# Performance work log

Measured on AMD Instinct MI355X. Metric: run time of the kernel, lower is better.

Reference implementation:

```python
import jax, jax.numpy as jnp
import numpy as np

EPS = 1e-5
D_MODEL, D_INNER, D_STATE, DT_RANK, D_CONV = 768, 1536, 16, 48, 4
B, T, FREQ, CLASSES = 4, 1000, 229, 88
MIDFEAT = 128 * (FREQ // 16)  # 1792


def conv2d_same(x, w):
    return jax.lax.conv_general_dilated(x, w, (1, 1), 'SAME',
                                        dimension_numbers=('NCHW', 'OIHW', 'NCHW'))


def bn2d_eval(h, g, b):
    # eval-mode BatchNorm2d with running_mean=0, running_var=1 (init values)
    s = g / jnp.sqrt(1.0 + EPS)
    return h * s[None, :, None, None] + b[None, :, None, None]


def conv_block(h, w1, g1, b1, w2, g2, b2):
    h = jax.nn.relu(bn2d_eval(conv2d_same(h, w1), g1, b1))
    h = jax.nn.relu(bn2d_eval(conv2d_same(h, w2), g2, b2))
    # avg_pool2d kernel (1,2), stride (1,2), floor mode -> VALID reduce_window
    h = jax.lax.reduce_window(h, 0.0, jax.lax.add, (1, 1, 1, 2), (1, 1, 1, 2), 'VALID')
    return h * 0.5


def mamba(x, in_w, conv_w, conv_b, xproj_w, dt_w, dt_b, A_log, Dp, out_w):
    Bb, L, _ = x.shape
    xz = x @ in_w.T                                  # (B,L,2*d_inner)
    xm, z = xz[..., :D_INNER], xz[..., D_INNER:]
    # depthwise causal conv1d, kernel 4, left pad 3
    xt = jax.lax.conv_general_dilated(xm.transpose(0, 2, 1), conv_w, (1,),
                                      [(D_CONV - 1, 0)],
                                      dimension_numbers=('NCH', 'OIH', 'NCH'),
                                      feature_group_count=D_INNER)
    xm = jax.nn.silu(xt.transpose(0, 2, 1) + conv_b)  # (B,L,d_inner)
    dbl = xm @ xproj_w.T                              # (B,L,dt_rank+2*d_state)
    dt = jax.nn.softplus(dbl[..., :DT_RANK] @ dt_w.T + dt_b)   # (B,L,d_inner)
    Bm = dbl[..., DT_RANK:DT_RANK + D_STATE]          # (B,L,N)
    Cm = dbl[..., DT_RANK + D_STATE:]                 # (B,L,N)
    A = -jnp.exp(A_log)                               # (d_inner,N)
    dA = jnp.exp(jnp.einsum('bld,dn->bldn', dt, A))   # (B,L,d_inner,N)
    dBx = jnp.einsum('bld,bln->bldn', dt * xm, Bm)    # (B,L,d_inner,N)

    def step(h, inp):
        a, bx, c = inp
        h = a * h + bx                                # (B,d_inner,N)
        return h, jnp.einsum('bdn,bn->bd', h, c)

    h0 = jnp.zeros((Bb, D_INNER, D_STATE), x.dtype)
    _, ys = jax.lax.scan(step, h0, (dA.transpose(1, 0, 2, 3),
                                    dBx.transpose(1, 0, 2, 3),
                                    Cm.transpose(1, 0, 2)))
    y = ys.transpose(1, 0, 2) + xm * Dp               # (B,L,d_inner)
    return (y * jax.nn.silu(z)) @ out_w.T             # (B,L,d_model)


def _forward(x,
             cb1_w1, cb1_g1, cb1_b1, cb1_w2, cb1_g2, cb1_b2,
             cb2_w1, cb2_g1, cb2_b1, cb2_w2, cb2_g2, cb2_b2,
             cb3_w1, cb3_g1, cb3_b1, cb3_w2, cb3_g2, cb3_b2,
             cb4_w1, cb4_g1, cb4_b1, cb4_w2, cb4_g2, cb4_b2,
             fc5_w, bn5_g, bn5_b, ln_g, ln_b,
             m_in_w, m_conv_w, m_conv_b, m_xproj_w, m_dt_w, m_dt_b,
             m_A_log, m_D, m_out_w, proj_w, proj_b):
    h = conv_block(x, cb1_w1, cb1_g1, cb1_b1, cb1_w2, cb1_g2, cb1_b2)
    h = conv_block(h, cb2_w1, cb2_g1, cb2_b1, cb2_w2, cb2_g2, cb2_b2)
    h = conv_block(h, cb3_w1, cb3_g1, cb3_b1, cb3_w2, cb3_g2, cb3_b2)
    h = conv_block(h, cb4_w1, cb4_g1, cb4_b1, cb4_w2, cb4_g2, cb4_b2)
    Bb, C, Tt, Fq = h.shape                           # (B,128,T,14)
    h = h.transpose(0, 2, 1, 3).reshape(Bb, Tt, C * Fq)  # torch transpose(1,2).flatten(2)
    # fc5 (bias=False) + eval BatchNorm1d(768) + relu
    h = jax.nn.relu((h @ fc5_w.T) * (bn5_g / jnp.sqrt(1.0 + EPS)) + bn5_b)
    mu = h.mean(-1, keepdims=True)
    var = ((h - mu) ** 2).mean(-1, keepdims=True)
    h = (h - mu) / jnp.sqrt(var + EPS) * ln_g + ln_b
    h = mamba(h, m_in_w, m_conv_w, m_conv_b, m_xproj_w, m_dt_w, m_dt_b,
              m_A_log, m_D, m_out_w)
    return jax.nn.sigmoid(h @ proj_w.T + proj_b)      # (B,T,classes)


def setup_inputs() -> dict:
    key = jax.random.key(0)
    ks = iter(jax.random.split(key, 64))

    def rn(shape, s=0.02):
        return jax.random.normal(next(ks), shape, jnp.float32) * s

    d = {'x': jax.random.normal(next(ks), (B, 1, T, FREQ), jnp.float32)}
    for i, (ci, co) in enumerate([(1, 48), (48, 64), (64, 96), (96, 128)], 1):
        d[f'cb{i}_w1'] = rn((co, ci, 3, 3), 0.1)
        d[f'cb{i}_g1'] = jnp.ones((co,), jnp.float32)
        d[f'cb{i}_b1'] = jnp.zeros((co,), jnp.float32)
        d[f'cb{i}_w2'] = rn((co, co, 3, 3), 0.05)
        d[f'cb{i}_g2'] = jnp.ones((co,), jnp.float32)
        d[f'cb{i}_b2'] = jnp.zeros((co,), jnp.float32)
    d['fc5_w'] = rn((D_MODEL, MIDFEAT))
    d['bn5_g'] = jnp.ones((D_MODEL,), jnp.float32)
    d['bn5_b'] = jnp.zeros((D_MODEL,), jnp.float32)
    d['ln_g'] = jnp.ones((D_MODEL,), jnp.float32)
    d['ln_b'] = jnp.zeros((D_MODEL,), jnp.float32)
    d['m_in_w'] = rn((2 * D_INNER, D_MODEL))
    d['m_conv_w'] = rn((D_INNER, 1, D_CONV), 0.1)
    d['m_conv_b'] = jnp.zeros((D_INNER,), jnp.float32)
    d['m_xproj_w'] = rn((DT_RANK + 2 * D_STATE, D_INNER))
    d['m_dt_w'] = rn((D_INNER, DT_RANK), 0.05)
    d['m_dt_b'] = jax.random.uniform(next(ks), (D_INNER,), jnp.float32, -6.0, -3.0)
    d['m_A_log'] = jnp.log(jnp.tile(jnp.arange(1, D_STATE + 1, dtype=jnp.float32)[None, :],
                                    (D_INNER, 1)))
    d['m_D'] = jnp.ones((D_INNER,), jnp.float32)
    d['m_out_w'] = rn((D_MODEL, D_INNER))
    d['proj_w'] = rn((CLASSES, D_MODEL))
    d['proj_b'] = jnp.zeros((CLASSES,), jnp.float32)
    return d


def reference(x,
              cb1_w1, cb1_g1, cb1_b1, cb1_w2, cb1_g2, cb1_b2,
              cb2_w1, cb2_g1, cb2_b1, cb2_w2, cb2_g2, cb2_b2,
              cb3_w1, cb3_g1, cb3_b1, cb3_w2, cb3_g2, cb3_b2,
              cb4_w1, cb4_g1, cb4_b1, cb4_w2, cb4_g2, cb4_b2,
              fc5_w, bn5_g, bn5_b, ln_g, ln_b,
              m_in_w, m_conv_w, m_conv_b, m_xproj_w, m_dt_w, m_dt_b,
              m_A_log, m_D, m_out_w, proj_w, proj_b):
    return _forward(x,
                    cb1_w1, cb1_g1, cb1_b1, cb1_w2, cb1_g2, cb1_b2,
                    cb2_w1, cb2_g1, cb2_b1, cb2_w2, cb2_g2, cb2_b2,
                    cb3_w1, cb3_g1, cb3_b1, cb3_w2, cb3_g2, cb3_b2,
                    cb4_w1, cb4_g1, cb4_b1, cb4_w2, cb4_g2, cb4_b2,
                    fc5_w, bn5_g, bn5_b, ln_g, ln_b,
                    m_in_w, m_conv_w, m_conv_b, m_xproj_w, m_dt_w, m_dt_b,
                    m_A_log, m_D, m_out_w, proj_w, proj_b)
```

## Files before the change

kernel.cpp:

```cpp
#include <hip/hip_runtime.h>
#include <math.h>


static __device__ __forceinline__ float sigmoidf_(float x) {
  return 1.f / (1.f + __expf(-x));
}
static __device__ __forceinline__ unsigned short f2bf(float f) {
  union { float f; unsigned int u; } c; c.f = f;
  unsigned int u = c.u;
  unsigned int r = (u + 0x7FFFu + ((u >> 16) & 1u)) >> 16;
  return (unsigned short)r;
}
static __device__ __forceinline__ float bf2f(unsigned short b) {
  union { unsigned int u; float f; } c; c.u = ((unsigned int)b) << 16;
  return c.f;
}
static __device__ __forceinline__ void glds16(const void* g, void* l) {
  __builtin_amdgcn_global_load_lds(
      (const __attribute__((address_space(1))) unsigned int*)g,
      (__attribute__((address_space(3))) unsigned int*)l, 16, 0, 0);
}

typedef __attribute__((ext_vector_type(8))) short short8b;
typedef __attribute__((ext_vector_type(4))) float f32x4;
typedef __attribute__((ext_vector_type(4))) unsigned short ushort4b;

__global__ __launch_bounds__(256)
void zero_border(unsigned short* __restrict__ buf, int F, int Cp, int total)
{
  int idx = blockIdx.x * 256 + threadIdx.x;
  if (idx >= total) return;
  int rowelems = (F + 2) * Cp;
  if (idx < 2 * rowelems) {
    int r = idx / rowelems;
    int k = idx % rowelems;
    buf[(size_t)(r * 1001) * rowelems + k] = 0;
  } else {
    int j = idx - 2 * rowelems;
    int t = j / (2 * Cp) + 1;
    int side = (j / Cp) & 1;
    int c = j % Cp;
    buf[((size_t)t * (F + 2) + (side ? F + 1 : 0)) * Cp + c] = 0;
  }
}

__global__ __launch_bounds__(256)
void wt_transform(const float* __restrict__ W, unsigned short* __restrict__ dst,
                  int CO, int CIN, int COp, int Cpin, int total)
{
  int idx = blockIdx.x * 256 + threadIdx.x;
  if (idx >= total) return;
  int ci = idx % Cpin;
  int co = (idx / Cpin) % COp;
  int s  = idx / (Cpin * COp);
  float v = (co < CO && ci < CIN) ? W[((size_t)co * CIN + ci) * 9 + s] : 0.f;
  dst[idx] = f2bf(v);
}

__global__ __launch_bounds__(256)
void wcvt(const float* __restrict__ src, unsigned short* __restrict__ dst, int total)
{
  int i = blockIdx.x * 256 + threadIdx.x;
  if (i < total) dst[i] = f2bf(src[i]);
}

__global__ __launch_bounds__(256)
void conv1_first(const float* __restrict__ x, const float* __restrict__ W,
                 const float* __restrict__ g, const float* __restrict__ bt,
                 unsigned short* __restrict__ out)
{
  __shared__ float ws[48 * 9];
  __shared__ float xs[3][6];
  const int tid = threadIdx.x;
  const int f0 = blockIdx.x * 4;
  const int t  = blockIdx.y;
  for (int i = tid; i < 48 * 9; i += 256) ws[i] = W[i];
  if (tid < 18) {
    int r = tid / 6, c = tid % 6;
    int ff = f0 - 1 + c, tt = t - 1 + r;
    xs[r][c] = (ff >= 0 && ff < 229 && tt >= 0 && tt < 1000)
                   ? x[tt * 229 + ff] : 0.f;
  }
  __syncthreads();
  const int co = tid & 63;
  const int fi = tid >> 6;
  const int f  = f0 + fi;
  float v = 0.f;
  if (co < 48) {
    float acc = 0.f;
    #pragma unroll
    for (int ky = 0; ky < 3; ++ky)
      #pragma unroll
      for (int kx = 0; kx < 3; ++kx)
        acc = fmaf(ws[co * 9 + ky * 3 + kx], xs[ky][fi + kx], acc);
    const float inv = rsqrtf(1.f + 1e-5f);
    v = fmaxf(fmaf(acc, g[co] * inv, bt[co]), 0.f);
  }
  if (f < 229)
    out[((size_t)(t + 1) * 231 + f + 1) * 64 + co] = f2bf(v);
}

template<int COp, int Cpin, int F, int BM, int CO>
__global__ __launch_bounds__(256)
void conv_mfma(const unsigned short* __restrict__ act,
               const unsigned short* __restrict__ W9,
               const float* __restrict__ gam, const float* __restrict__ bet,
               unsigned short* __restrict__ out, int M)
{
  static_assert(BM == 64 || BM == 128, "");
  constexpr int MI = BM / 32;
  constexpr int NJ = COp / 32;
  constexpr int KSTEPS = Cpin / 32;
  __shared__ alignas(16) short A_s[4 * BM * 8];
  __shared__ alignas(16) short B_s[4 * COp * 8];

  const int tid  = threadIdx.x;
  const int lane = tid & 63, w = tid >> 6;
  const int wm = w >> 1, wn = w & 1;
  const int m0 = blockIdx.x * BM;
  const int wbase = tid & 192;

  int prA[BM / 64];
  #pragma unroll
  for (int j = 0; j < BM / 64; ++j) {
    int slot = j * 256 + tid;
    int row  = slot % BM;
    int pos  = m0 + row; if (pos >= M) pos = M - 1;
    int t = pos / F, f = pos - t * F;
    prA[j] = (t + 1) * (F + 2) + (f + 1);
  }

  f32x4 acc[MI][NJ];
  #pragma unroll
  for (int i = 0; i < MI; ++i)
    #pragma unroll
    for (int jn = 0; jn < NJ; ++jn) acc[i][jn] = (f32x4){0.f, 0.f, 0.f, 0.f};

  for (int s = 0; s < 9; ++s) {
    const int soff = (s / 3 - 1) * (F + 2) + (s % 3) - 1;
    for (int kc = 0; kc < KSTEPS; ++kc) {
      __syncthreads();
      #pragma unroll
      for (int j = 0; j < BM / 64; ++j) {
        int slot = j * 256 + tid;
        int q = slot / BM;
        glds16(&act[(size_t)(prA[j] + soff) * Cpin + kc * 32 + q * 8],
               &A_s[(j * 256 + wbase) * 8]);
      }
      #pragma unroll
      for (int sb = 0; sb < (COp * 4 + 255) / 256; ++sb) {
        int slot = sb * 256 + tid;
        if (slot < COp * 4) {
          int q = slot / COp, co = slot % COp;
          glds16(&W9[((size_t)(s * COp + co)) * Cpin + kc * 32 + q * 8],
                 &B_s[(sb * 256 + wbase) * 8]);
        }
      }
      __syncthreads();
      const int lr = lane & 15, lq = lane >> 4;
      short8b a[MI], b[NJ];
      #pragma unroll
      for (int i = 0; i < MI; ++i)
        a[i] = *(const short8b*)&A_s[(lq * BM + wm * (BM / 2) + i * 16 + lr) * 8];
      #pragma unroll
      for (int jn = 0; jn < NJ; ++jn)
        b[jn] = *(const short8b*)&B_s[(lq * COp + wn * (COp / 2) + jn * 16 + lr) * 8];
      #pragma unroll
      for (int i = 0; i < MI; ++i)
        #pragma unroll
        for (int jn = 0; jn < NJ; ++jn)
          acc[i][jn] = __builtin_amdgcn_mfma_f32_16x16x32_bf16(
              a[i], b[jn], acc[i][jn], 0, 0, 0);
    }
  }
  const float inv = rsqrtf(1.f + 1e-5f);
  const int lr = lane & 15, lq = lane >> 4;
  #pragma unroll
  for (int jn = 0; jn < NJ; ++jn) {
    int co = wn * (COp / 2) + jn * 16 + lr;
    float sc = (co < CO) ? gam[co] * inv : 0.f;
    float bi = (co < CO) ? bet[co] : 0.f;
    #pragma unroll
    for (int i = 0; i < MI; ++i) {
      #pragma unroll
      for (int r = 0; r < 4; ++r) {
        int pos = m0 + wm * (BM / 2) + i * 16 + lq * 4 + r;
        if (pos < M) {
          int t = pos / F, f = pos - t * F;
          float v = fmaxf(fmaf(acc[i][jn][r], sc, bi), 0.f);
          out[((size_t)(t + 1) * (F + 2) + f + 1) * COp + co] = f2bf(v);
        }
      }
    }
  }
}

__global__ __launch_bounds__(256)
void pool_ch(const unsigned short* __restrict__ in, unsigned short* __restrict__ out,
             int Fin, int Fo, int Cp, int total4)
{
  int idx = blockIdx.x * 256 + threadIdx.x;
  if (idx >= total4) return;
  int cg = Cp / 4;
  int c4 = idx % cg;
  int fo = (idx / cg) % Fo;
  int t  = idx / (cg * Fo);
  size_t bi = ((size_t)(t + 1) * (Fin + 2) + 2 * fo + 1) * Cp + c4 * 4;
  ushort4b a = *(const ushort4b*)&in[bi];
  ushort4b b = *(const ushort4b*)&in[bi + Cp];
  ushort4b o;
  #pragma unroll
  for (int e = 0; e < 4; ++e)
    o[e] = f2bf((bf2f(a[e]) + bf2f(b[e])) * 0.5f);
  *(ushort4b*)&out[((size_t)(t + 1) * (Fo + 2) + fo + 1) * Cp + c4 * 4] = o;
}

__global__ __launch_bounds__(256)
void pool4_trans(const unsigned short* __restrict__ in,
                 unsigned short* __restrict__ feat, int boff)
{
  int idx = blockIdx.x * 256 + threadIdx.x;
  if (idx >= 1000 * 128 * 14) return;
  int fo = idx % 14;
  int co = (idx / 14) % 128;
  int t  = idx / (14 * 128);
  size_t bi = ((size_t)(t + 1) * 30 + 2 * fo + 1) * 128 + co;
  float v = (bf2f(in[bi]) + bf2f(in[bi + 128])) * 0.5f;
  feat[((size_t)(boff + t)) * 1792 + co * 14 + fo] = f2bf(v);
}

template<int EPI>
__global__ __launch_bounds__(256)
void gemm_bf16(const unsigned short* __restrict__ A, int lda,
               const unsigned short* __restrict__ W, float* __restrict__ C,
               int M, int N, int K,
               const float* __restrict__ sc, const float* __restrict__ bi)
{
  __shared__ alignas(16) short A_s[4 * 128 * 8];
  __shared__ alignas(16) short B_s[4 * 64 * 8];
  const int tid  = threadIdx.x;
  const int lane = tid & 63, w = tid >> 6;
  const int wm = w >> 1, wn = w & 1;
  const int m0 = blockIdx.y * 128, n0 = blockIdx.x * 64;
  const int wbase = tid & 192;

  int mrow[2];
  #pragma unroll
  for (int j = 0; j < 2; ++j) {
    int slot = j * 256 + tid;
    int row = slot & 127;
    int m = m0 + row; if (m >= M) m = M - 1;
    mrow[j] = m;
  }
  const int bq = tid >> 6, bn = tid & 63;

  f32x4 acc[4][2];
  #pragma unroll
  for (int i = 0; i < 4; ++i)
    #pragma unroll
    for (int jn = 0; jn < 2; ++jn) acc[i][jn] = (f32x4){0.f, 0.f, 0.f, 0.f};

  for (int k0 = 0; k0 < K; k0 += 32) {
    __syncthreads();
    #pragma unroll
    for (int j = 0; j < 2; ++j) {
      int slot = j * 256 + tid;
      int q = slot >> 7;
      glds16(&A[(size_t)mrow[j] * lda + k0 + q * 8],
             &A_s[(j * 256 + wbase) * 8]);
    }
    glds16(&W[(size_t)(n0 + bn) * K + k0 + bq * 8], &B_s[wbase * 8]);
    __syncthreads();
    const int lr = lane & 15, lq = lane >> 4;
    short8b a[4], b[2];
    #pragma unroll
    for (int i = 0; i < 4; ++i)
      a[i] = *(const short8b*)&A_s[(lq * 128 + wm * 64 + i * 16 + lr) * 8];
    #pragma unroll
    for (int jn = 0; jn < 2; ++jn)
      b[jn] = *(const short8b*)&B_s[(lq * 64 + wn * 32 + jn * 16 + lr) * 8];
    #pragma unroll
    for (int i = 0; i < 4; ++i)
      #pragma unroll
      for (int jn = 0; jn < 2; ++jn)
        acc[i][jn] = __builtin_amdgcn_mfma_f32_16x16x32_bf16(
            a[i], b[jn], acc[i][jn], 0, 0, 0);
  }
  const float inv = rsqrtf(1.f + 1e-5f);
  const int lr = lane & 15, lq = lane >> 4;
  #pragma unroll
  for (int jn = 0; jn < 2; ++jn) {
    int col = n0 + wn * 32 + jn * 16 + lr;
    float scv = (EPI == 1) ? sc[col] * inv : 0.f;
    float biv = (EPI == 1) ? bi[col] : 0.f;
    #pragma unroll
    for (int i = 0; i < 4; ++i) {
      #pragma unroll
      for (int r = 0; r < 4; ++r) {
        int row = m0 + wm * 64 + i * 16 + lq * 4 + r;
        if (row < M) {
          float v = acc[i][jn][r];
          if (EPI == 1) v = fmaxf(fmaf(v, scv, biv), 0.f);
          C[(size_t)row * N + col] = v;
        }
      }
    }
  }
}

template<int EPI>
__global__ __launch_bounds__(256)
void gemm_nt(const float* __restrict__ A, int lda,
             const float* __restrict__ W,
             float* __restrict__ C, int M, int N, int K,
             const float* __restrict__ sc, const float* __restrict__ bi)
{
  __shared__ float As[16][68];
  __shared__ float Bs[16][68];
  const int tid = threadIdx.x;
  const int m0 = blockIdx.y * 64, n0 = blockIdx.x * 64;
  const int tx = tid % 16, ty = tid / 16;
  const int lr = tid / 4, lk = (tid % 4) * 4;
  float acc[4][4];
  #pragma unroll
  for (int i = 0; i < 4; ++i)
    #pragma unroll
    for (int j = 0; j < 4; ++j) acc[i][j] = 0.f;

  for (int k0 = 0; k0 < K; k0 += 16) {
    __syncthreads();
    {
      int m = m0 + lr;
      float4 a = make_float4(0.f, 0.f, 0.f, 0.f);
      if (m < M) a = *(const float4*)(A + (size_t)m * lda + k0 + lk);
      As[lk + 0][lr] = a.x; As[lk + 1][lr] = a.y;
      As[lk + 2][lr] = a.z; As[lk + 3][lr] = a.w;
      int n = n0 + lr;
      float4 wv = make_float4(0.f, 0.f, 0.f, 0.f);
      if (n < N) wv = *(const float4*)(W + (size_t)n * K + k0 + lk);
      Bs[lk + 0][lr] = wv.x; Bs[lk + 1][lr] = wv.y;
      Bs[lk + 2][lr] = wv.z; Bs[lk + 3][lr] = wv.w;
    }
    __syncthreads();
    #pragma unroll
    for (int kk = 0; kk < 16; ++kk) {
      float4 av = *(const float4*)(&As[kk][ty * 4]);
      float4 bv = *(const float4*)(&Bs[kk][tx * 4]);
      float a[4] = {av.x, av.y, av.z, av.w};
      float bb[4] = {bv.x, bv.y, bv.z, bv.w};
      #pragma unroll
      for (int i = 0; i < 4; ++i)
        #pragma unroll
        for (int j = 0; j < 4; ++j)
          acc[i][j] = fmaf(a[i], bb[j], acc[i][j]);
    }
  }
  #pragma unroll
  for (int i = 0; i < 4; ++i) {
    int m = m0 + ty * 4 + i;
    if (m >= M) continue;
    #pragma unroll
    for (int j = 0; j < 4; ++j) {
      int n = n0 + tx * 4 + j;
      if (n >= N) continue;
      float v = acc[i][j];
      if (EPI == 2) {
        float x = v + bi[n];
        v = (x > 20.f) ? x : log1pf(__expf(x));
      } else if (EPI == 3) {
        v = sigmoidf_(v + bi[n]);
      }
      C[(size_t)m * N + n] = v;
    }
  }
}

__global__ __launch_bounds__(256)
void layernorm768_bf(const float* __restrict__ in, const float* __restrict__ g,
                     const float* __restrict__ b, unsigned short* __restrict__ out)
{
  const int row = blockIdx.x;
  const float* x = in + (size_t)row * 768;
  const int tid = threadIdx.x;
  float v0 = x[tid], v1 = x[tid + 256], v2 = x[tid + 512];
  float s = v0 + v1 + v2;
  float q = v0 * v0 + v1 * v1 + v2 * v2;
  #pragma unroll
  for (int off = 32; off >= 1; off >>= 1) {
    s += __shfl_down(s, off);
    q += __shfl_down(q, off);
  }
  __shared__ float rs[4], rq[4];
  int wave = tid >> 6;
  if ((tid & 63) == 0) { rs[wave] = s; rq[wave] = q; }
  __syncthreads();
  float ts = rs[0] + rs[1] + rs[2] + rs[3];
  float tq = rq[0] + rq[1] + rq[2] + rq[3];
  float mu = ts * (1.f / 768.f);
  float var = tq * (1.f / 768.f) - mu * mu;
  float rstd = rsqrtf(var + 1e-5f);
  unsigned short* o = out + (size_t)row * 768;
  o[tid]       = f2bf((v0 - mu) * rstd * g[tid]       + b[tid]);
  o[tid + 256] = f2bf((v1 - mu) * rstd * g[tid + 256] + b[tid + 256]);
  o[tid + 512] = f2bf((v2 - mu) * rstd * g[tid + 512] + b[tid + 512]);
}

__global__ __launch_bounds__(256)
void dwconv_silu(const float* __restrict__ xz, const float* __restrict__ cw,
                 const float* __restrict__ cb, float* __restrict__ xmc, int total)
{
  int idx = blockIdx.x * 256 + threadIdx.x;
  if (idx >= total) return;
  int d = idx % 1536;
  int t = (idx / 1536) % 1000;
  int b = idx / (1536 * 1000);
  float acc = cb[d];
  #pragma unroll
  for (int j = 0; j < 4; ++j) {
    int tt = t - 3 + j;
    if (tt >= 0)
      acc = fmaf(cw[d * 4 + j], xz[((size_t)(b * 1000 + tt)) * 3072 + d], acc);
  }
  xmc[idx] = acc * sigmoidf_(acc);
}

__global__ __launch_bounds__(64)
void scan_p1(const float* __restrict__ dt, const float* __restrict__ xmc,
             const float* __restrict__ dbl, const float* __restrict__ A_log,
             float* __restrict__ hend, float* __restrict__ pend)
{
  const int d = blockIdx.x * 64 + threadIdx.x;
  const int b = blockIdx.y;
  const int c = blockIdx.z;
  float A[16], h[16];
  #pragma unroll
  for (int n = 0; n < 16; ++n) {
    A[n] = -__expf(A_log[d * 16 + n]);
    h[n] = 0.f;
  }
  float S = 0.f;
  const int t0 = c * 125;
  for (int t = t0; t < t0 + 125; ++t) {
    size_t r = (size_t)b * 1000 + t;
    float dtv = dt[r * 1536 + d];
    float xv  = xmc[r * 1536 + d];
    const float* bc = dbl + r * 80;
    float dtx = dtv * xv;
    S += dtv;
    #pragma unroll
    for (int n = 0; n < 16; ++n)
      h[n] = fmaf(__expf(dtv * A[n]), h[n], dtx * bc[48 + n]);
  }
  size_t base = (((size_t)c * 4 + b) * 1536 + d) * 16;
  #pragma unroll
  for (int n = 0; n < 16; ++n) {
    hend[base + n] = h[n];
    pend[base + n] = __expf(S * A[n]);
  }
}

__global__ __launch_bounds__(256)
void scan_p2(const float* __restrict__ hend, const float* __restrict__ pend,
             float* __restrict__ hin)
{
  int gid = blockIdx.x * 256 + threadIdx.x;
  if (gid >= 6144) return;
  float cur[16];
  #pragma unroll
  for (int n = 0; n < 16; ++n) cur[n] = 0.f;
  for (int c = 0; c < 8; ++c) {
    size_t base = ((size_t)c * 6144 + gid) * 16;
    #pragma unroll
    for (int n = 0; n < 16; ++n) {
      hin[base + n] = cur[n];
      cur[n] = fmaf(pend[base + n], cur[n], hend[base + n]);
    }
  }
}

__global__ __launch_bounds__(64)
void scan_p3(const float* __restrict__ dt, const float* __restrict__ xmc,
             const float* __restrict__ dbl, const float* __restrict__ xz,
             const float* __restrict__ A_log, const float* __restrict__ Dp,
             const float* __restrict__ hin, unsigned short* __restrict__ g_out)
{
  const int d = blockIdx.x * 64 + threadIdx.x;
  const int b = blockIdx.y;
  const int c = blockIdx.z;
  float A[16], h[16];
  size_t base = (((size_t)c * 4 + b) * 1536 + d) * 16;
  #pragma unroll
  for (int n = 0; n < 16; ++n) {
    A[n] = -__expf(A_log[d * 16 + n]);
    h[n] = hin[base + n];
  }
  const float Dd = Dp[d];
  const int t0 = c * 125;
  for (int t = t0; t < t0 + 125; ++t) {
    size_t r = (size_t)b * 1000 + t;
    float dtv = dt[r * 1536 + d];
    float xv  = xmc[r * 1536 + d];
    float zv  = xz[r * 3072 + 1536 + d];
    const float* bc = dbl + r * 80;
    float dtx = dtv * xv;
    float y = 0.f;
    #pragma unroll
    for (int n = 0; n < 16; ++n) {
      float hn = fmaf(__expf(dtv * A[n]), h[n], dtx * bc[48 + n]);
      h[n] = hn;
      y = fmaf(hn, bc[64 + n], y);
    }
    y = fmaf(xv, Dd, y);
    g_out[r * 1536 + d] = f2bf(y * (zv * sigmoidf_(zv)));
  }
}

extern "C" void kernel_launch(void* const* d_in, const int* in_sizes, int n_in,
                              void* d_out, int out_size, void* d_ws, size_t ws_size,
                              hipStream_t stream)
{
  const float* x    = (const float*)d_in[0];
  const float* cw1[4] = {(const float*)d_in[1],  (const float*)d_in[7],
                         (const float*)d_in[13], (const float*)d_in[19]};
  const float* cg1[4] = {(const float*)d_in[2],  (const float*)d_in[8],
                         (const float*)d_in[14], (const float*)d_in[20]};
  const float* cb1[4] = {(const float*)d_in[3],  (const float*)d_in[9],
                         (const float*)d_in[15], (const float*)d_in[21]};
  const float* cw2[4] = {(const float*)d_in[4],  (const float*)d_in[10],
                         (const float*)d_in[16], (const float*)d_in[22]};
  const float* cg2[4] = {(const float*)d_in[5],  (const float*)d_in[11],
                         (const float*)d_in[17], (const float*)d_in[23]};
  const float* cb2[4] = {(const float*)d_in[6],  (const float*)d_in[12],
                         (const float*)d_in[18], (const float*)d_in[24]};
  const float* fc5w = (const float*)d_in[25]; const float* bn5g = (const float*)d_in[26]; const float* bn5b = (const float*)d_in[27];
  const float* lng  = (const float*)d_in[28]; const float* lnb  = (const float*)d_in[29];
  const float* minw = (const float*)d_in[30]; const float* mcw  = (const float*)d_in[31]; const float* mcb  = (const float*)d_in[32];
  const float* mxw  = (const float*)d_in[33]; const float* mdtw = (const float*)d_in[34]; const float* mdtb = (const float*)d_in[35];
  const float* malog= (const float*)d_in[36]; const float* mD   = (const float*)d_in[37]; const float* moutw= (const float*)d_in[38];
  const float* pw   = (const float*)d_in[39]; const float* pb   = (const float*)d_in[40];

  char* ws = (char*)d_ws;
  unsigned short* bufA = (unsigned short*)(ws + 0);
  unsigned short* bufB = (unsigned short*)(ws + 30000000);
  unsigned short* w1b = (unsigned short*)(ws + 60000000);
  unsigned short* w2a = (unsigned short*)(ws + 60100000);
  unsigned short* w2b = (unsigned short*)(ws + 60200000);
  unsigned short* w3a = (unsigned short*)(ws + 60300000);
  unsigned short* w3b = (unsigned short*)(ws + 60450000);
  unsigned short* w4a = (unsigned short*)(ws + 60650000);
  unsigned short* w4b = (unsigned short*)(ws + 60900000);
  unsigned short* fc5w_bf = (unsigned short*)(ws + 61500000);
  unsigned short* minw_bf = (unsigned short*)(ws + 64300000);
  unsigned short* feat_bf = (unsigned short*)(ws + 69100000);
  float*          hfc     = (float*)(ws + 83500000);
  unsigned short* hln     = (unsigned short*)(ws + 95900000);
  unsigned short* moutw_bf= (unsigned short*)(ws + 102200000);
  float*          hend    = (float*)(ws + 104700000);
  float*          pend    = (float*)(ws + 107900000);
  float*          hin     = (float*)(ws + 111100000);
  unsigned short* gbf     = (unsigned short*)(ws + 114300000);
  float* xzb  = (float*)(ws + 0);
  float* xmc  = (float*)(ws + 49200000);
  float* dblb = (float*)(ws + 74000000);
  float* dtb  = (float*)(ws + 75500000);
  float* mam  = (float*)(ws + 83500000);

  dim3 blk(256);

  {
    struct WT { const float* src; unsigned short* dst; int CO, CIN, COp, Cpin; };
    WT wt[7] = {
      {cw2[0], w1b,  48,  48,  64,  64},
      {cw1[1], w2a,  64,  48,  64,  64},
      {cw2[1], w2b,  64,  64,  64,  64},
      {cw1[2], w3a,  96,  64,  96,  64},
      {cw2[2], w3b,  96,  96,  96,  96},
      {cw1[3], w4a, 128,  96, 128,  96},
      {cw2[3], w4b, 128, 128, 128, 128},
    };
    for (int i = 0; i < 7; ++i) {
      int total = 9 * wt[i].COp * wt[i].Cpin;
      wt_transform<<<dim3((total + 255) / 256), blk, 0, stream>>>(
          wt[i].src, wt[i].dst, wt[i].CO, wt[i].CIN, wt[i].COp, wt[i].Cpin, total);
    }
    wcvt<<<dim3((1376256 + 255) / 256), blk, 0, stream>>>(fc5w, fc5w_bf, 1376256);
    wcvt<<<dim3((2359296 + 255) / 256), blk, 0, stream>>>(minw, minw_bf, 2359296);
    wcvt<<<dim3((1179648 + 255) / 256), blk, 0, stream>>>(moutw, moutw_bf, 1179648);
  }

  auto zb = [&](unsigned short* buf, int F, int Cp) {
    int total = 2 * (F + 2) * Cp + 2000 * Cp;
    zero_border<<<dim3((total + 255) / 256), blk, 0, stream>>>(buf, F, Cp, total);
  };
  auto pool = [&](const unsigned short* in, unsigned short* out,
                  int Fin, int Fo, int Cp) {
    int total4 = 1000 * Fo * Cp / 4;
    pool_ch<<<dim3((total4 + 255) / 256), blk, 0, stream>>>(in, out, Fin, Fo, Cp, total4);
  };

  for (int b = 0; b < 4; ++b) {
    const float* xb = x + (size_t)b * 1000 * 229;
    zb(bufA, 229, 64);
    conv1_first<<<dim3(58, 1000), blk, 0, stream>>>(xb, cw1[0], cg1[0], cb1[0], bufA);
    zb(bufB, 229, 64);
    conv_mfma<64, 64, 229, 128, 48><<<dim3(1790), blk, 0, stream>>>(
        bufA, w1b, cg2[0], cb2[0], bufB, 229000);
    zb(bufA, 114, 64);
    pool(bufB, bufA, 229, 114, 64);
    zb(bufB, 114, 64);
    conv_mfma<64, 64, 114, 128, 64><<<dim3(891), blk, 0, stream>>>(
        bufA, w2a, cg1[1], cb1[1], bufB, 114000);
    zb(bufA, 114, 64);
    conv_mfma<64, 64, 114, 128, 64><<<dim3(891), blk, 0, stream>>>(
        bufB, w2b, cg2[1], cb2[1], bufA, 114000);
    zb(bufB, 57, 64);
    pool(bufA, bufB, 114, 57, 64);
    zb(bufA, 57, 96);
    conv_mfma<96, 64, 57, 128, 96><<<dim3(446), blk, 0, stream>>>(
        bufB, w3a, cg1[2], cb1[2], bufA, 57000);
    zb(bufB, 57, 96);
    conv_mfma<96, 96, 57, 128, 96><<<dim3(446), blk, 0, stream>>>(
        bufA, w3b, cg2[2], cb2[2], bufB, 57000);
    zb(bufA, 28, 96);
    pool(bufB, bufA, 57, 28, 96);
    zb(bufB, 28, 128);
    conv_mfma<128, 96, 28, 64, 128><<<dim3(438), blk, 0, stream>>>(
        bufA, w4a, cg1[3], cb1[3], bufB, 28000);
    zb(bufA, 28, 128);
    conv_mfma<128, 128, 28, 64, 128><<<dim3(438), blk, 0, stream>>>(
        bufB, w4b, cg2[3], cb2[3], bufA, 28000);
    pool4_trans<<<dim3((1000 * 128 * 14 + 255) / 256), blk, 0, stream>>>(
        bufA, feat_bf, b * 1000);
  }

  gemm_bf16<1><<<dim3(12, 32), blk, 0, stream>>>(feat_bf, 1792, fc5w_bf, hfc, 4000, 768, 1792, bn5g, bn5b);
  layernorm768_bf<<<dim3(4000), blk, 0, stream>>>(hfc, lng, lnb, hln);
  gemm_bf16<0><<<dim3(48, 32), blk, 0, stream>>>(hln, 768, minw_bf, xzb, 4000, 3072, 768, nullptr, nullptr);
  dwconv_silu<<<dim3((6144000 + 255) / 256), blk, 0, stream>>>(xzb, mcw, mcb, xmc, 6144000);
  gemm_nt<0><<<dim3(2, 63), blk, 0, stream>>>(xmc, 1536, mxw, dblb, 4000, 80, 1536, nullptr, nullptr);
  gemm_nt<2><<<dim3(24, 63), blk, 0, stream>>>(dblb, 80, mdtw, dtb, 4000, 1536, 48, nullptr, mdtb);
  scan_p1<<<dim3(24, 4, 8), dim3(64), 0, stream>>>(dtb, xmc, dblb, malog, hend, pend);
  scan_p2<<<dim3(24), blk, 0, stream>>>(hend, pend, hin);
  scan_p3<<<dim3(24, 4, 8), dim3(64), 0, stream>>>(dtb, xmc, dblb, xzb, malog, mD, hin, gbf);
  gemm_bf16<0><<<dim3(12, 32), blk, 0, stream>>>(gbf, 1536, moutw_bf, mam, 4000, 768, 1536, nullptr, nullptr);
  gemm_nt<3><<<dim3(2, 63), blk, 0, stream>>>(mam, 768, pw, (float*)d_out, 4000, 88, 768, nullptr, pb);
}
```

Baseline: 2.108 ms.

## Batch conv stages across batch via grid z and move small GEMMs to bf16 MFMA

Layers 2-4 of the conv stack now run once over all four batch items, using a grid z dimension and per-batch buffer strides, instead of in a per-batch loop. Border zeroing is hoisted to a few up-front launches. The fp32 SIMT gemm_nt kernels for x_proj, dt_proj and the output projection are replaced with the bf16 MFMA gemm, using padded bf16 weights and extra bf16 output copies. The goal is fewer launches, larger grids for better occupancy, and matrix-core use for the small GEMMs. In exchange the workspace is remapped with heavy buffer aliasing, and these GEMMs now run at bf16 precision.

```diff
diff --git a/kernel.cpp b/kernel.cpp
--- a/kernel.cpp
+++ b/kernel.cpp
@@ -26,21 +26,25 @@
 typedef __attribute__((ext_vector_type(4))) unsigned short ushort4b;
 
 __global__ __launch_bounds__(256)
-void zero_border(unsigned short* __restrict__ buf, int F, int Cp, int total)
+void zero_border(unsigned short* __restrict__ buf, int F, int Cp, int totalPB,
+                 int nb, int bstride)
 {
   int idx = blockIdx.x * 256 + threadIdx.x;
-  if (idx >= total) return;
+  if (idx >= totalPB * nb) return;
+  int b = idx / totalPB;
+  int k = idx % totalPB;
+  unsigned short* p = buf + (size_t)b * bstride;
   int rowelems = (F + 2) * Cp;
-  if (idx < 2 * rowelems) {
-    int r = idx / rowelems;
-    int k = idx % rowelems;
-    buf[(size_t)(r * 1001) * rowelems + k] = 0;
+  if (k < 2 * rowelems) {
+    int r = k / rowelems;
+    int e = k % rowelems;
+    p[(size_t)(r * 1001) * rowelems + e] = 0;
   } else {
-    int j = idx - 2 * rowelems;
+    int j = k - 2 * rowelems;
     int t = j / (2 * Cp) + 1;
     int side = (j / Cp) & 1;
     int c = j % Cp;
-    buf[((size_t)t * (F + 2) + (side ? F + 1 : 0)) * Cp + c] = 0;
+    p[((size_t)t * (F + 2) + (side ? F + 1 : 0)) * Cp + c] = 0;
   }
 }
 
@@ -62,6 +66,24 @@
 {
   int i = blockIdx.x * 256 + threadIdx.x;
   if (i < total) dst[i] = f2bf(src[i]);
+}
+__global__ __launch_bounds__(256)
+void wpadN(const float* __restrict__ src, unsigned short* __restrict__ dst,
+           int Nreal, int Npad, int K)
+{
+  int idx = blockIdx.x * 256 + threadIdx.x;
+  if (idx >= Npad * K) return;
+  int n = idx / K, k = idx % K;
+  dst[idx] = (n < Nreal) ? f2bf(src[(size_t)n * K + k]) : 0;
+}
+__global__ __launch_bounds__(256)
+void wpadK(const float* __restrict__ src, unsigned short* __restrict__ dst,
+           int Kreal, int Kpad, int N)
+{
+  int idx = blockIdx.x * 256 + threadIdx.x;
+  if (idx >= N * Kpad) return;
+  int n = idx / Kpad, k = idx % Kpad;
+  dst[idx] = (k < Kreal) ? f2bf(src[(size_t)n * Kreal + k]) : 0;
 }
 
 __global__ __launch_bounds__(256)
@@ -102,10 +124,11 @@
 
 template<int COp, int Cpin, int F, int BM, int CO>
 __global__ __launch_bounds__(256)
-void conv_mfma(const unsigned short* __restrict__ act,
+void conv_mfma(const unsigned short* __restrict__ act0,
                const unsigned short* __restrict__ W9,
                const float* __restrict__ gam, const float* __restrict__ bet,
-               unsigned short* __restrict__ out, int M)
+               unsigned short* __restrict__ out0, int M,
+               int actStride, int outStride)
 {
   static_assert(BM == 64 || BM == 128, "");
   constexpr int MI = BM / 32;
@@ -113,6 +136,9 @@
   constexpr int KSTEPS = Cpin / 32;
   __shared__ alignas(16) short A_s[4 * BM * 8];
   __shared__ alignas(16) short B_s[4 * COp * 8];
+
+  const unsigned short* act = act0 + (size_t)blockIdx.z * actStride;
+  unsigned short* out = out0 + (size_t)blockIdx.z * outStride;
 
   const int tid  = threadIdx.x;
   const int lane = tid & 63, w = tid >> 6;
@@ -196,11 +222,13 @@
 }
 
 __global__ __launch_bounds__(256)
-void pool_ch(const unsigned short* __restrict__ in, unsigned short* __restrict__ out,
-             int Fin, int Fo, int Cp, int total4)
+void pool_ch(const unsigned short* __restrict__ in0, unsigned short* __restrict__ out0,
+             int Fin, int Fo, int Cp, int total4, int inStride, int outStride)
 {
   int idx = blockIdx.x * 256 + threadIdx.x;
   if (idx >= total4) return;
+  const unsigned short* in = in0 + (size_t)blockIdx.z * inStride;
+  unsigned short* out = out0 + (size_t)blockIdx.z * outStride;
   int cg = Cp / 4;
   int c4 = idx % cg;
   int fo = (idx / cg) % Fo;
@@ -216,11 +244,13 @@
 }
 
 __global__ __launch_bounds__(256)
-void pool4_trans(const unsigned short* __restrict__ in,
-                 unsigned short* __restrict__ feat, int boff)
+void pool4_trans(const unsigned short* __restrict__ in0,
+                 unsigned short* __restrict__ feat, int inStride)
 {
   int idx = blockIdx.x * 256 + threadIdx.x;
   if (idx >= 1000 * 128 * 14) return;
+  const unsigned short* in = in0 + (size_t)blockIdx.z * inStride;
+  int boff = blockIdx.z * 1000;
   int fo = idx % 14;
   int co = (idx / 14) % 128;
   int t  = idx / (14 * 128);
@@ -229,11 +259,12 @@
   feat[((size_t)(boff + t)) * 1792 + co * 14 + fo] = f2bf(v);
 }
 
-template<int EPI>
+template<int EPI, bool OUTF32, bool OUTBF>
 __global__ __launch_bounds__(256)
 void gemm_bf16(const unsigned short* __restrict__ A, int lda,
-               const unsigned short* __restrict__ W, float* __restrict__ C,
-               int M, int N, int K,
+               const unsigned short* __restrict__ W,
+               float* __restrict__ C, unsigned short* __restrict__ Cbf,
+               int M, int Nout, int ldc, int K,
                const float* __restrict__ sc, const float* __restrict__ bi)
 {
   __shared__ alignas(16) short A_s[4 * 128 * 8];
@@ -291,8 +322,9 @@
   #pragma unroll
   for (int jn = 0; jn < 2; ++jn) {
     int col = n0 + wn * 32 + jn * 16 + lr;
+    if (col >= Nout) continue;
     float scv = (EPI == 1) ? sc[col] * inv : 0.f;
-    float biv = (EPI == 1) ? bi[col] : 0.f;
+    float biv = (EPI == 1 || EPI == 2 || EPI == 3) ? (bi ? bi[col] : 0.f) : 0.f;
     #pragma unroll
     for (int i = 0; i < 4; ++i) {
       #pragma unroll
@@ -301,76 +333,16 @@
         if (row < M) {
           float v = acc[i][jn][r];
           if (EPI == 1) v = fmaxf(fmaf(v, scv, biv), 0.f);
-          C[(size_t)row * N + col] = v;
+          else if (EPI == 2) {
+            float xx = v + biv;
+            v = (xx > 20.f) ? xx : log1pf(__expf(xx));
+          } else if (EPI == 3) {
+            v = sigmoidf_(v + biv);
+          }
+          if (OUTF32) C[(size_t)row * ldc + col] = v;
+          if (OUTBF)  Cbf[(size_t)row * ldc + col] = f2bf(v);
         }
       }
-    }
-  }
-}
-
-template<int EPI>
-__global__ __launch_bounds__(256)
-void gemm_nt(const float* __restrict__ A, int lda,
-             const float* __restrict__ W,
-             float* __restrict__ C, int M, int N, int K,
-             const float* __restrict__ sc, const float* __restrict__ bi)
-{
-  __shared__ float As[16][68];
-  __shared__ float Bs[16][68];
-  const int tid = threadIdx.x;
-  const int m0 = blockIdx.y * 64, n0 = blockIdx.x * 64;
-  const int tx = tid % 16, ty = tid / 16;
-  const int lr = tid / 4, lk = (tid % 4) * 4;
-  float acc[4][4];
-  #pragma unroll
-  for (int i = 0; i < 4; ++i)
-    #pragma unroll
-    for (int j = 0; j < 4; ++j) acc[i][j] = 0.f;
-
-  for (int k0 = 0; k0 < K; k0 += 16) {
-    __syncthreads();
-    {
-      int m = m0 + lr;
-      float4 a = make_float4(0.f, 0.f, 0.f, 0.f);
-      if (m < M) a = *(const float4*)(A + (size_t)m * lda + k0 + lk);
-      As[lk + 0][lr] = a.x; As[lk + 1][lr] = a.y;
-      As[lk + 2][lr] = a.z; As[lk + 3][lr] = a.w;
-      int n = n0 + lr;
-      float4 wv = make_float4(0.f, 0.f, 0.f, 0.f);
-      if (n < N) wv = *(const float4*)(W + (size_t)n * K + k0 + lk);
-      Bs[lk + 0][lr] = wv.x; Bs[lk + 1][lr] = wv.y;
-      Bs[lk + 2][lr] = wv.z; Bs[lk + 3][lr] = wv.w;
-    }
-    __syncthreads();
-    #pragma unroll
-    for (int kk = 0; kk < 16; ++kk) {
-      float4 av = *(const float4*)(&As[kk][ty * 4]);
-      float4 bv = *(const float4*)(&Bs[kk][tx * 4]);
-      float a[4] = {av.x, av.y, av.z, av.w};
-      float bb[4] = {bv.x, bv.y, bv.z, bv.w};
-      #pragma unroll
-      for (int i = 0; i < 4; ++i)
-        #pragma unroll
-        for (int j = 0; j < 4; ++j)
-          acc[i][j] = fmaf(a[i], bb[j], acc[i][j]);
-    }
-  }
-  #pragma unroll
-  for (int i = 0; i < 4; ++i) {
-    int m = m0 + ty * 4 + i;
-    if (m >= M) continue;
-    #pragma unroll
-    for (int j = 0; j < 4; ++j) {
-      int n = n0 + tx * 4 + j;
-      if (n >= N) continue;
-      float v = acc[i][j];
-      if (EPI == 2) {
-        float x = v + bi[n];
-        v = (x > 20.f) ? x : log1pf(__expf(x));
-      } else if (EPI == 3) {
-        v = sigmoidf_(v + bi[n]);
-      }
-      C[(size_t)m * N + n] = v;
     }
   }
 }
@@ -407,7 +379,8 @@
 
 __global__ __launch_bounds__(256)
 void dwconv_silu(const float* __restrict__ xz, const float* __restrict__ cw,
-                 const float* __restrict__ cb, float* __restrict__ xmc, int total)
+                 const float* __restrict__ cb, float* __restrict__ xmc,
+                 unsigned short* __restrict__ xmc_bf, int total)
 {
   int idx = blockIdx.x * 256 + threadIdx.x;
   if (idx >= total) return;
@@ -421,7 +394,9 @@
     if (tt >= 0)
       acc = fmaf(cw[d * 4 + j], xz[((size_t)(b * 1000 + tt)) * 3072 + d], acc);
   }
-  xmc[idx] = acc * sigmoidf_(acc);
+  float v = acc * sigmoidf_(acc);
+  xmc[idx] = v;
+  xmc_bf[idx] = f2bf(v);
 }
 
 __global__ __launch_bounds__(64)
@@ -444,7 +419,7 @@
     size_t r = (size_t)b * 1000 + t;
     float dtv = dt[r * 1536 + d];
     float xv  = xmc[r * 1536 + d];
-    const float* bc = dbl + r * 80;
+    const float* bc = dbl + r * 128;
     float dtx = dtv * xv;
     S += dtv;
     #pragma unroll
@@ -501,7 +476,7 @@
     float dtv = dt[r * 1536 + d];
     float xv  = xmc[r * 1536 + d];
     float zv  = xz[r * 3072 + 1536 + d];
-    const float* bc = dbl + r * 80;
+    const float* bc = dbl + r * 128;
     float dtx = dtv * xv;
     float y = 0.f;
     #pragma unroll
@@ -540,30 +515,49 @@
   const float* pw   = (const float*)d_in[39]; const float* pb   = (const float*)d_in[40];
 
   char* ws = (char*)d_ws;
-  unsigned short* bufA = (unsigned short*)(ws + 0);
-  unsigned short* bufB = (unsigned short*)(ws + 30000000);
-  unsigned short* w1b = (unsigned short*)(ws + 60000000);
-  unsigned short* w2a = (unsigned short*)(ws + 60100000);
-  unsigned short* w2b = (unsigned short*)(ws + 60200000);
-  unsigned short* w3a = (unsigned short*)(ws + 60300000);
-  unsigned short* w3b = (unsigned short*)(ws + 60450000);
-  unsigned short* w4a = (unsigned short*)(ws + 60650000);
-  unsigned short* w4b = (unsigned short*)(ws + 60900000);
-  unsigned short* fc5w_bf = (unsigned short*)(ws + 61500000);
-  unsigned short* minw_bf = (unsigned short*)(ws + 64300000);
-  unsigned short* feat_bf = (unsigned short*)(ws + 69100000);
-  float*          hfc     = (float*)(ws + 83500000);
-  unsigned short* hln     = (unsigned short*)(ws + 95900000);
-  unsigned short* moutw_bf= (unsigned short*)(ws + 102200000);
-  float*          hend    = (float*)(ws + 104700000);
-  float*          pend    = (float*)(ws + 107900000);
-  float*          hin     = (float*)(ws + 111100000);
-  unsigned short* gbf     = (unsigned short*)(ws + 114300000);
-  float* xzb  = (float*)(ws + 0);
-  float* xmc  = (float*)(ws + 49200000);
-  float* dblb = (float*)(ws + 74000000);
-  float* dtb  = (float*)(ws + 75500000);
-  float* mam  = (float*)(ws + 83500000);
+  const int S1 = 1002 * 116 * 64;
+  const int S2 = 1002 * 59 * 64;
+  const int S3 = 1002 * 59 * 96;
+  const int S4 = 1002 * 30 * 96;
+  const int S5 = 1002 * 30 * 128;
+  unsigned short* bufA   = (unsigned short*)(ws + 0);
+  unsigned short* bufB   = (unsigned short*)(ws + 29700000);
+  unsigned short* P1out  = (unsigned short*)(ws + 60000000);
+  unsigned short* L2buf  = (unsigned short*)(ws + 0);
+  unsigned short* L2bufB = (unsigned short*)(ws + 60000000);
+  unsigned short* P2out  = (unsigned short*)(ws + 0);
+  unsigned short* L3buf  = (unsigned short*)(ws + 31000000);
+  unsigned short* L3buf2 = (unsigned short*)(ws + 76500000);
+  unsigned short* P3out  = (unsigned short*)(ws + 0);
+  unsigned short* L4buf  = (unsigned short*)(ws + 24000000);
+  unsigned short* L4buf2 = (unsigned short*)(ws + 55000000);
+  unsigned short* w1b = (unsigned short*)(ws + 122000000);
+  unsigned short* w2a = (unsigned short*)(ws + 122100000);
+  unsigned short* w2b = (unsigned short*)(ws + 122200000);
+  unsigned short* w3a = (unsigned short*)(ws + 122300000);
+  unsigned short* w3b = (unsigned short*)(ws + 122450000);
+  unsigned short* w4a = (unsigned short*)(ws + 122650000);
+  unsigned short* w4b = (unsigned short*)(ws + 122900000);
+  unsigned short* feat_bf = (unsigned short*)(ws + 86000000);
+  float*          hfc      = (float*)(ws + 0);
+  float*          xzb      = (float*)(ws + 0);
+  float*          xmc      = (float*)(ws + 49200000);
+  unsigned short* minw_bf  = (unsigned short*)(ws + 73800000);
+  unsigned short* hln      = (unsigned short*)(ws + 78600000);
+  float*          dtb      = (float*)(ws + 73800000);
+  unsigned short* xmc_bf   = (unsigned short*)(ws + 98400000);
+  unsigned short* gbf      = (unsigned short*)(ws + 98400000);
+  float*          dblb     = (float*)(ws + 110700000);
+  unsigned short* dblb_bf  = (unsigned short*)(ws + 112800000);
+  unsigned short* dtw_bf   = (unsigned short*)(ws + 113900000);
+  float*          hend     = (float*)(ws + 113900000);
+  unsigned short* mam_bf   = (unsigned short*)(ws + 113900000);
+  unsigned short* xprojw_bf= (unsigned short*)(ws + 117100000);
+  float*          pend     = (float*)(ws + 117100000);
+  unsigned short* fc5w_bf  = (unsigned short*)(ws + 120300000);
+  float*          hin      = (float*)(ws + 120300000);
+  unsigned short* moutw_bf = (unsigned short*)(ws + 123500000);
+  unsigned short* pw_bf    = (unsigned short*)(ws + 125900000);
 
   dim3 blk(256);
 
@@ -583,65 +577,73 @@
       wt_transform<<<dim3((total + 255) / 256), blk, 0, stream>>>(
           wt[i].src, wt[i].dst, wt[i].CO, wt[i].CIN, wt[i].COp, wt[i].Cpin, total);
     }
-    wcvt<<<dim3((1376256 + 255) / 256), blk, 0, stream>>>(fc5w, fc5w_bf, 1376256);
-    wcvt<<<dim3((2359296 + 255) / 256), blk, 0, stream>>>(minw, minw_bf, 2359296);
-    wcvt<<<dim3((1179648 + 255) / 256), blk, 0, stream>>>(moutw, moutw_bf, 1179648);
-  }
-
-  auto zb = [&](unsigned short* buf, int F, int Cp) {
-    int total = 2 * (F + 2) * Cp + 2000 * Cp;
-    zero_border<<<dim3((total + 255) / 256), blk, 0, stream>>>(buf, F, Cp, total);
+  }
+
+  auto zb = [&](unsigned short* buf, int F, int Cp, int nb, int bstride) {
+    int totalPB = 2 * (F + 2) * Cp + 2000 * Cp;
+    zero_border<<<dim3((totalPB * nb + 255) / 256), blk, 0, stream>>>(
+        buf, F, Cp, totalPB, nb, bstride);
   };
-  auto pool = [&](const unsigned short* in, unsigned short* out,
-                  int Fin, int Fo, int Cp) {
-    int total4 = 1000 * Fo * Cp / 4;
-    pool_ch<<<dim3((total4 + 255) / 256), blk, 0, stream>>>(in, out, Fin, Fo, Cp, total4);
-  };
+
+  zb(bufA,  229, 64, 1, 0);
+  zb(P1out, 114, 64, 4, S1);
+  zb(L2buf, 114, 64, 4, S1);
+  zb(P2out,  57, 64, 4, S2);
+  zb(L3buf,  57, 96, 4, S3);
+  zb(P3out,  28, 96, 4, S4);
+  zb(L4buf,  28, 128, 4, S5);
 
   for (int b = 0; b < 4; ++b) {
     const float* xb = x + (size_t)b * 1000 * 229;
-    zb(bufA, 229, 64);
     conv1_first<<<dim3(58, 1000), blk, 0, stream>>>(xb, cw1[0], cg1[0], cb1[0], bufA);
-    zb(bufB, 229, 64);
     conv_mfma<64, 64, 229, 128, 48><<<dim3(1790), blk, 0, stream>>>(
-        bufA, w1b, cg2[0], cb2[0], bufB, 229000);
-    zb(bufA, 114, 64);
-    pool(bufB, bufA, 229, 114, 64);
-    zb(bufB, 114, 64);
-    conv_mfma<64, 64, 114, 128, 64><<<dim3(891), blk, 0, stream>>>(
-        bufA, w2a, cg1[1], cb1[1], bufB, 114000);
-    zb(bufA, 114, 64);
-    conv_mfma<64, 64, 114, 128, 64><<<dim3(891), blk, 0, stream>>>(
-        bufB, w2b, cg2[1], cb2[1], bufA, 114000);
-    zb(bufB, 57, 64);
-    pool(bufA, bufB, 114, 57, 64);
-    zb(bufA, 57, 96);
-    conv_mfma<96, 64, 57, 128, 96><<<dim3(446), blk, 0, stream>>>(
-        bufB, w3a, cg1[2], cb1[2], bufA, 57000);
-    zb(bufB, 57, 96);
-    conv_mfma<96, 96, 57, 128, 96><<<dim3(446), blk, 0, stream>>>(
-        bufA, w3b, cg2[2], cb2[2], bufB, 57000);
-    zb(bufA, 28, 96);
-    pool(bufB, bufA, 57, 28, 96);
-    zb(bufB, 28, 128);
-    conv_mfma<128, 96, 28, 64, 128><<<dim3(438), blk, 0, stream>>>(
-        bufA, w4a, cg1[3], cb1[3], bufB, 28000);
-    zb(bufA, 28, 128);
-    conv_mfma<128, 128, 28, 64, 128><<<dim3(438), blk, 0, stream>>>(
-        bufB, w4b, cg2[3], cb2[3], bufA, 28000);
-    pool4_trans<<<dim3((1000 * 128 * 14 + 255) / 256), blk, 0, stream>>>(
-        bufA, feat_bf, b * 1000);
-  }
-
-  gemm_bf16<1><<<dim3(12, 32), blk, 0, stream>>>(feat_bf, 1792, fc5w_bf, hfc, 4000, 768, 1792, bn5g, bn5b);
+        bufA, w1b, cg2[0], cb2[0], bufB, 229000, 0, 0);
+    pool_ch<<<dim3((1000 * 114 * 64 / 4 + 255) / 256), blk, 0, stream>>>(
+        bufB, P1out + (size_t)b * S1, 229, 114, 64, 1000 * 114 * 64 / 4, 0, 0);
+  }
+
+  conv_mfma<64, 64, 114, 128, 64><<<dim3(891, 1, 4), blk, 0, stream>>>(
+      P1out, w2a, cg1[1], cb1[1], L2buf, 114000, S1, S1);
+  conv_mfma<64, 64, 114, 128, 64><<<dim3(891, 1, 4), blk, 0, stream>>>(
+      L2buf, w2b, cg2[1], cb2[1], L2bufB, 114000, S1, S1);
+  pool_ch<<<dim3((1000 * 57 * 64 / 4 + 255) / 256, 1, 4), blk, 0, stream>>>(
+      L2bufB, P2out, 114, 57, 64, 1000 * 57 * 64 / 4, S1, S2);
+  conv_mfma<96, 64, 57, 128, 96><<<dim3(446, 1, 4), blk, 0, stream>>>(
+      P2out, w3a, cg1[2], cb1[2], L3buf, 57000, S2, S3);
+  conv_mfma<96, 96, 57, 128, 96><<<dim3(446, 1, 4), blk, 0, stream>>>(
+      L3buf, w3b, cg2[2], cb2[2], L3buf2, 57000, S3, S3);
+  pool_ch<<<dim3((1000 * 28 * 96 / 4 + 255) / 256, 1, 4), blk, 0, stream>>>(
+      L3buf2, P3out, 57, 28, 96, 1000 * 28 * 96 / 4, S3, S4);
+  conv_mfma<128, 96, 28, 64, 128><<<dim3(438, 1, 4), blk, 0, stream>>>(
+      P3out, w4a, cg1[3], cb1[3], L4buf, 28000, S4, S5);
+  conv_mfma<128, 128, 28, 64, 128><<<dim3(438, 1, 4), blk, 0, stream>>>(
+      L4buf, w4b, cg2[3], cb2[3], L4buf2, 28000, S5, S5);
+  pool4_trans<<<dim3((1000 * 128 * 14 + 255) / 256, 1, 4), blk, 0, stream>>>(
+      L4buf2, feat_bf, S5);
+
+  wcvt<<<dim3((1376256 + 255) / 256), blk, 0, stream>>>(fc5w, fc5w_bf, 1376256);
+  wcvt<<<dim3((2359296 + 255) / 256), blk, 0, stream>>>(minw, minw_bf, 2359296);
+  wcvt<<<dim3((1179648 + 255) / 256), blk, 0, stream>>>(moutw, moutw_bf, 1179648);
+  wpadN<<<dim3((128 * 1536 + 255) / 256), blk, 0, stream>>>(mxw, xprojw_bf, 80, 128, 1536);
+  wpadK<<<dim3((1536 * 64 + 255) / 256), blk, 0, stream>>>(mdtw, dtw_bf, 48, 64, 1536);
+  wpadN<<<dim3((128 * 768 + 255) / 256), blk, 0, stream>>>(pw, pw_bf, 88, 128, 768);
+
+  gemm_bf16<1, true, false><<<dim3(12, 32), blk, 0, stream>>>(
+      feat_bf, 1792, fc5w_bf, hfc, nullptr, 4000, 768, 768, 1792, bn5g, bn5b);
   layernorm768_bf<<<dim3(4000), blk, 0, stream>>>(hfc, lng, lnb, hln);
-  gemm_bf16<0><<<dim3(48, 32), blk, 0, stream>>>(hln, 768, minw_bf, xzb, 4000, 3072, 768, nullptr, nullptr);
-  dwconv_silu<<<dim3((6144000 + 255) / 256), blk, 0, stream>>>(xzb, mcw, mcb, xmc, 6144000);
-  gemm_nt<0><<<dim3(2, 63), blk, 0, stream>>>(xmc, 1536, mxw, dblb, 4000, 80, 1536, nullptr, nullptr);
-  gemm_nt<2><<<dim3(24, 63), blk, 0, stream>>>(dblb, 80, mdtw, dtb, 4000, 1536, 48, nullptr, mdtb);
+  gemm_bf16<0, true, false><<<dim3(48, 32), blk, 0, stream>>>(
+      hln, 768, minw_bf, xzb, nullptr, 4000, 3072, 3072, 768, nullptr, nullptr);
+  dwconv_silu<<<dim3((6144000 + 255) / 256), blk, 0, stream>>>(
+      xzb, mcw, mcb, xmc, xmc_bf, 6144000);
+  gemm_bf16<0, true, true><<<dim3(2, 32), blk, 0, stream>>>(
+      xmc_bf, 1536, xprojw_bf, dblb, dblb_bf, 4000, 128, 128, 1536, nullptr, nullptr);
+  gemm_bf16<2, true, false><<<dim3(24, 32), blk, 0, stream>>>(
+      dblb_bf, 128, dtw_bf, dtb, nullptr, 4000, 1536, 1536, 64, nullptr, mdtb);
   scan_p1<<<dim3(24, 4, 8), dim3(64), 0, stream>>>(dtb, xmc, dblb, malog, hend, pend);
   scan_p2<<<dim3(24), blk, 0, stream>>>(hend, pend, hin);
   scan_p3<<<dim3(24, 4, 8), dim3(64), 0, stream>>>(dtb, xmc, dblb, xzb, malog, mD, hin, gbf);
-  gemm_bf16<0><<<dim3(12, 32), blk, 0, stream>>>(gbf, 1536, moutw_bf, mam, 4000, 768, 1536, nullptr, nullptr);
-  gemm_nt<3><<<dim3(2, 63), blk, 0, stream>>>(mam, 768, pw, (float*)d_out, 4000, 88, 768, nullptr, pb);
-}
+  gemm_bf16<0, false, true><<<dim3(12, 32), blk, 0, stream>>>(
+      gbf, 1536, moutw_bf, nullptr, mam_bf, 4000, 768, 768, 1536, nullptr, nullptr);
+  gemm_bf16<3, true, false><<<dim3(2, 32), blk, 0, stream>>>(
+      mam_bf, 768, pw_bf, (float*)d_out, nullptr, 4000, 88, 88, 768, nullptr, pb);
+}
```

New measurement: 1.739 ms. -17.5%, faster.
